# Performance work log

Measured on AMD Instinct MI355X. Metric: run time of the kernel, lower is better.

The kernel has to match this reference:

```python
import math
import jax, jax.numpy as jnp
import numpy as np

D_MODEL = 1024
N_HEAD = 16
HEAD_DIM = D_MODEL // N_HEAD
MAX_LENGTH = 2048


def sinusoid_table():
    # Matches RelativeEmbedding.get_embedding with num_embeddings = max_length + 1
    num_emb = MAX_LENGTH + 1
    half = HEAD_DIM // 2
    freq = jnp.exp(jnp.arange(half, dtype=jnp.float32) * (-math.log(10000.0) / (half - 1)))
    lo = -((num_emb + 1) // 2)  # python floor of -num_emb//2
    hi = num_emb // 2
    pos = jnp.arange(lo, hi, dtype=jnp.float32)  # length num_emb
    ang = pos[:, None] * freq[None, :]
    table = jnp.concatenate([jnp.sin(ang), jnp.cos(ang)], axis=1)  # (num_emb, HEAD_DIM)
    origin_shift = num_emb // 2 + 1
    return table, origin_shift


def _shift(BD):
    # (b, n, L, 2L) -> (b, n, L, L) diagonal-shift trick
    b, n, L, _ = BD.shape
    BD = jnp.concatenate([BD, jnp.zeros((b, n, L, 1), BD.dtype)], axis=-1)
    BD = BD.reshape(b, n, -1, L)[:, :, :-1, :].reshape(b, n, L, -1)
    return BD[:, :, :, :L]


def setup_inputs() -> dict:
    key = jax.random.key(0)
    k1, k2, k3, k4 = jax.random.split(key, 4)
    B, L = 2, 1024
    x = jax.random.normal(k1, (B, L, D_MODEL), dtype=jnp.float32)
    mask = jnp.ones((B, L), dtype=jnp.int32)
    W_qv = jax.random.normal(k2, (2 * D_MODEL, D_MODEL), dtype=jnp.float32) * 0.02
    r_r_bias = jax.random.normal(k3, (N_HEAD, HEAD_DIM), dtype=jnp.float32) * 0.02
    r_w_bias = jax.random.normal(k4, (N_HEAD, HEAD_DIM), dtype=jnp.float32) * 0.02
    return {"x": x, "mask": mask, "W_qv": W_qv, "r_r_bias": r_r_bias, "r_w_bias": r_w_bias}


def reference(x, mask, W_qv, r_r_bias, r_w_bias):
    B, L, d = x.shape
    table, origin_shift = sinusoid_table()
    pos = jnp.arange(-L, L) + origin_shift
    pos_embed = table[pos]  # (2L, head_dim)

    qv = x @ W_qv.T  # (B, L, 2d)
    q, v = jnp.split(qv, 2, axis=-1)
    q = q.reshape(B, L, N_HEAD, HEAD_DIM).transpose(0, 2, 1, 3)  # (B,H,L,dh)
    k = x.reshape(B, L, N_HEAD, HEAD_DIM).transpose(0, 2, 1, 3)
    v = v.reshape(B, L, N_HEAD, HEAD_DIM).transpose(0, 2, 1, 3)

    AC = jnp.einsum('bnqd,bnkd->bnqk', q + r_r_bias[None, :, None, :], k)
    D_ = jnp.einsum('nd,ld->nl', r_w_bias, pos_embed)[None, :, None, :]  # (1,H,1,2L)
    B_ = jnp.einsum('bnqd,ld->bnql', q, pos_embed)  # (B,H,L,2L)
    BD = _shift(B_ + D_)

    attn = AC + BD
    attn = jnp.where(mask[:, None, None, :] == 0, -jnp.inf, attn)
    attn = jax.nn.softmax(attn, axis=-1)
    out = jnp.einsum('bnqk,bnkd->bnqd', attn, v)
    return out.transpose(0, 2, 1, 3).reshape(B, L, d)
```

## Files before the change

### kernel.cpp

```cpp
#include <hip/hip_runtime.h>
#include <hip/hip_bf16.h>
#include <math.h>

#define L_SEQ 1024
#define TWO_L 2048
#define NHEAD 16
#define HD 64
#define DM 1024
#define BATCH 2
#define PE2R 2176
#define GBS 132

typedef _Float16 f16;
typedef _Float16 f16x4 __attribute__((ext_vector_type(4)));
typedef _Float16 f16x8 __attribute__((ext_vector_type(8)));
typedef float f32x4 __attribute__((ext_vector_type(4)));

__device__ __forceinline__ f16x8 ld8(const f16* p) {
  f16x4 lo = *(const f16x4*)p;
  f16x4 hi = *(const f16x4*)(p + 16);
  f16x8 r;
  r[0] = lo[0]; r[1] = lo[1]; r[2] = lo[2]; r[3] = lo[3];
  r[4] = hi[0]; r[5] = hi[1]; r[6] = hi[2]; r[7] = hi[3];
  return r;
}

__device__ __forceinline__ float pe_val(int j, int d) {
  float posval = (float)(j - L_SEQ);
  float freq = expf(-(float)(d & 31) * 0.2971077539347156f);
  float ang = posval * freq;
  return (d < 32) ? sinf(ang) : cosf(ang);
}

__global__ __launch_bounds__(256) void prep1(const float* __restrict__ x,
                                             const float* __restrict__ W,
                                             f16* __restrict__ pe2,
                                             f16* __restrict__ xh,
                                             f16* __restrict__ Wh) {
  int bid = blockIdx.x, tid = threadIdx.x;
  if (bid < 2048) {
    int i = (bid * 256 + tid) * 4;
    float4 v = *(const float4*)(x + i);
    f16x4 o = {(f16)v.x, (f16)v.y, (f16)v.z, (f16)v.w};
    *(f16x4*)(xh + i) = o;
  } else if (bid < 4096) {
    int i = ((bid - 2048) * 256 + tid) * 4;
    float4 v = *(const float4*)(W + i);
    f16x4 o = {(f16)v.x, (f16)v.y, (f16)v.z, (f16)v.w};
    *(f16x4*)(Wh + i) = o;
  } else {
    int idx = (bid - 4096) * 256 + tid;
    int rrow = idx >> 6, d = idx & 63;
    int u = rrow - 1088;
    int j = (u < 0) ? u + 2049 : u;
    float v = (j != 2048) ? pe_val(j, d) : 0.f;
    pe2[idx] = (f16)v;
  }
}

__global__ __launch_bounds__(256) void prep2(const float* __restrict__ rr,
                                             const float* __restrict__ rw,
                                             const f16* __restrict__ pe2,
                                             float* __restrict__ D2x) {
  int idx = blockIdx.x * 256 + threadIdx.x;
  int h = idx / PE2R, r0 = idx - h * PE2R;
  float s = 0.f;
#pragma unroll
  for (int d = 0; d < HD; ++d)
    s = fmaf(rw[h * HD + d] - rr[h * HD + d], (float)pe2[r0 * HD + d], s);
  D2x[idx] = s;
}

#define QV_STEP(T, AS, BS, CA0, CA1, CB0, CB1, NA0, NA1, NB0, NB1)             \
  {                                                                            \
    *(f16x8*)&AS[r * 72 + c] = CA0;                                            \
    *(f16x8*)&AS[r * 72 + c + 8] = CA1;                                        \
    *(f16x8*)&BS[r * 72 + c] = CB0;                                            \
    *(f16x8*)&BS[r * 72 + c + 8] = CB1;                                        \
    __syncthreads();                                                           \
    if ((T) + 1 < 16) {                                                        \
      const f16* na = ga + ((T) + 1) * 64;                                     \
      NA0 = *(const f16x8*)na;                                                 \
      NA1 = *(const f16x8*)(na + 8);                                           \
      const f16* nb = gb + ((T) + 1) * 64;                                     \
      NB0 = *(const f16x8*)nb;                                                 \
      NB1 = *(const f16x8*)(nb + 8);                                           \
    }                                                                          \
    _Pragma("unroll")                                                          \
    for (int kc = 0; kc < 2; ++kc) {                                           \
      f16x8 a = ld8(&AS[(w * 16 + li) * 72 + kc * 32 + g * 4]);                \
      _Pragma("unroll")                                                        \
      for (int nf = 0; nf < 4; ++nf) {                                         \
        f16x8 bfr = ld8(&BS[(nf * 16 + li) * 72 + kc * 32 + g * 4]);           \
        s[nf] = __builtin_amdgcn_mfma_f32_16x16x32_f16(a, bfr, s[nf], 0, 0, 0);\
      }                                                                        \
    }                                                                          \
  }

__global__ __launch_bounds__(256) void qv_mfma(const f16* __restrict__ xh,
                                               const f16* __restrict__ Wh,
                                               f16* __restrict__ qvh,
                                               f16* __restrict__ vT) {
  __shared__ f16 As0[64 * 72], As1[64 * 72];
  __shared__ f16 Bs0[64 * 72], Bs1[64 * 72];
  int tid = threadIdx.x;
  int w = tid >> 6, lane = tid & 63, g = lane >> 4, li = lane & 15;
  int m0 = blockIdx.y * 64, n0 = blockIdx.x * 64;
  int r = tid >> 2, c = (tid & 3) * 16;

  const f16* ga = xh + (size_t)(m0 + r) * 1024 + c;
  const f16* gb = Wh + (size_t)(n0 + r) * 1024 + c;
  f16x8 ca0 = *(const f16x8*)ga, ca1 = *(const f16x8*)(ga + 8);
  f16x8 cb0 = *(const f16x8*)gb, cb1 = *(const f16x8*)(gb + 8);
  f16x8 na0, na1, nb0, nb1;

  f32x4 s[4];
#pragma unroll
  for (int i = 0; i < 4; ++i) s[i] = {0.f, 0.f, 0.f, 0.f};

  for (int t = 0; t < 16; t += 2) {
    QV_STEP(t, As0, Bs0, ca0, ca1, cb0, cb1, na0, na1, nb0, nb1);
    QV_STEP(t + 1, As1, Bs1, na0, na1, nb0, nb1, ca0, ca1, cb0, cb1);
  }

#pragma unroll
  for (int nf = 0; nf < 4; ++nf) {
    int n = n0 + nf * 16 + li;
#pragma unroll
    for (int rr2 = 0; rr2 < 4; ++rr2) {
      int m = m0 + w * 16 + g * 4 + rr2;
      f16 val = (f16)s[nf][rr2];
      if (n < 1024) {
        qvh[(size_t)m * 2048 + n] = val;
      } else {
        int b_ = m >> 10, ls = m & 1023, hd = n - 1024;
        vT[((size_t)(b_ * 16 + (hd >> 6)) * 64 + (hd & 63)) * 1024 + ls] = val;
      }
    }
  }
}

#define BANDFILL(TT, QOFF, PEREG, D2V)                                         \
  {                                                                            \
    _Pragma("unroll")                                                          \
    for (int qf = 0; qf < 4; ++qf) {                                           \
      f32x4 gacc = {0.f, 0.f, 0.f, 0.f};                                       \
      _Pragma("unroll")                                                        \
      for (int kc = 0; kc < 2; ++kc) {                                         \
        f16x8 qo = ld8(&Qs[((QOFF) + qf * 16 + li) * 72 + kc * 32 + g * 4]);   \
        gacc = __builtin_amdgcn_mfma_f32_16x16x32_f16(PEREG[kc], qo, gacc, 0, 0, 0); \
      }                                                                        \
      f16x4 gpk;                                                               \
      gpk[0] = (f16)(gacc[0] + (D2V).x); gpk[1] = (f16)(gacc[1] + (D2V).y);    \
      gpk[2] = (f16)(gacc[2] + (D2V).z); gpk[3] = (f16)(gacc[3] + (D2V).w);    \
      *(f16x4*)&Gb[(qf * 16 + li) * GBS + (TT) + w * 16 + g * 4] = gpk;        \
    }                                                                          \
  }

#define ATTN_STEP(T, CK0, CK1, CV0, CV1, NK0, NK1, NV0, NV1, CPE, NPE)         \
  {                                                                            \
    const int k0 = (T) * 64;                                                   \
    const int tt = (64 * (T)) & 127;                                           \
    const int qoff = (64 * (T) >= q0) ? 1 : 0;                                 \
    *(f16x8*)&Ks[r * 72 + c] = CK0;                                            \
    *(f16x8*)&Ks[r * 72 + c + 8] = CK1;                                        \
    *(f16x8*)&Vs[r * 72 + c] = CV0;                                            \
    *(f16x8*)&Vs[r * 72 + c + 8] = CV1;                                        \
    float4 d2v = *(const float4*)(D2x + hD2 + 1088 + k0 - q0 + w * 16 + g * 4);\
    BANDFILL(tt, qoff, CPE, d2v)                                               \
    __syncthreads();                                                           \
    if ((T) + 1 < 16) {                                                        \
      const f16* nk = gk + (size_t)((T) + 1) * 64 * 1024;                      \
      NK0 = *(const f16x8*)nk;                                                 \
      NK1 = *(const f16x8*)(nk + 8);                                           \
      const f16* nv = gv + ((T) + 1) * 64;                                     \
      NV0 = *(const f16x8*)nv;                                                 \
      NV1 = *(const f16x8*)(nv + 8);                                           \
      const f16* pb = pe2 + (size_t)(1088 + 64 * ((T) + 1) - q0 + w * 16 + li) * 64; \
      NPE[0] = ld8(pb + g * 4);                                                \
      NPE[1] = ld8(pb + 32 + g * 4);                                           \
    }                                                                          \
    float gf[16];                                                              \
    {                                                                          \
      const int cb0 = tt + g * 4 - qi + 128;                                   \
      _Pragma("unroll")                                                        \
      for (int kf = 0; kf < 4; ++kf)                                           \
        _Pragma("unroll")                                                      \
        for (int u2 = 0; u2 < 4; ++u2)                                         \
          gf[kf * 4 + u2] = (float)Gb[qi * GBS + ((cb0 + kf * 16 + u2) & 127)];\
    }                                                                          \
    f32x4 s[4];                                                                \
    _Pragma("unroll")                                                          \
    for (int i = 0; i < 4; ++i) s[i] = {0.f, 0.f, 0.f, 0.f};                   \
    __builtin_amdgcn_s_setprio(1);                                             \
    _Pragma("unroll")                                                          \
    for (int kc = 0; kc < 2; ++kc) {                                           \
      f16x8 qb = ld8(&Qs[(1 + w * 16 + li) * 72 + kc * 32 + g * 4]);           \
      _Pragma("unroll")                                                        \
      for (int kf = 0; kf < 4; ++kf) {                                         \
        f16x8 ka = ld8(&Ks[(kf * 16 + li) * 72 + kc * 32 + g * 4]);            \
        s[kf] = __builtin_amdgcn_mfma_f32_16x16x32_f16(ka, qb, s[kf], 0, 0, 0);\
      }                                                                        \
    }                                                                          \
    __builtin_amdgcn_s_setprio(0);                                             \
    float sv[16];                                                              \
    float tmax = -1e30f;                                                       \
    _Pragma("unroll")                                                          \
    for (int kf = 0; kf < 4; ++kf) {                                           \
      _Pragma("unroll")                                                        \
      for (int rr2 = 0; rr2 < 4; ++rr2) {                                      \
        float v_ = s[kf][rr2] + gf[kf * 4 + rr2] +                             \
                   Ms[k0 + kf * 16 + g * 4 + rr2];                             \
        sv[kf * 4 + rr2] = v_;                                                 \
        tmax = fmaxf(tmax, v_);                                                \
      }                                                                        \
    }                                                                          \
    tmax = fmaxf(tmax, __shfl_xor(tmax, 16));                                  \
    tmax = fmaxf(tmax, __shfl_xor(tmax, 32));                                  \
    if (!__all(tmax <= m_run + 8.f)) {                                         \
      float mnew = fmaxf(m_run, tmax);                                         \
      float scale = __expf(m_run - mnew);                                      \
      m_run = mnew;                                                            \
      l_run *= scale;                                                          \
      _Pragma("unroll")                                                        \
      for (int f = 0; f < 4; ++f) {                                            \
        o[f][0] *= scale; o[f][1] *= scale; o[f][2] *= scale; o[f][3] *= scale;\
      }                                                                        \
    }                                                                          \
    float pf[16];                                                              \
    float lloc = 0.f;                                                          \
    _Pragma("unroll")                                                          \
    for (int i = 0; i < 16; ++i) { pf[i] = __expf(sv[i] - m_run); lloc += pf[i]; } \
    l_run += lloc;                                                             \
    f16x8 pb0, pb1;                                                            \
    _Pragma("unroll")                                                          \
    for (int i = 0; i < 8; ++i) { pb0[i] = (f16)pf[i]; pb1[i] = (f16)pf[8 + i]; } \
    __builtin_amdgcn_s_setprio(1);                                             \
    _Pragma("unroll")                                                          \
    for (int f = 0; f < 4; ++f) {                                              \
      f16x8 va0 = ld8(&Vs[(f * 16 + li) * 72 + g * 4]);                        \
      o[f] = __builtin_amdgcn_mfma_f32_16x16x32_f16(va0, pb0, o[f], 0, 0, 0);  \
      f16x8 va1 = ld8(&Vs[(f * 16 + li) * 72 + 32 + g * 4]);                   \
      o[f] = __builtin_amdgcn_mfma_f32_16x16x32_f16(va1, pb1, o[f], 0, 0, 0);  \
    }                                                                          \
    __builtin_amdgcn_s_setprio(0);                                             \
    __syncthreads();                                                           \
  }

__global__ __launch_bounds__(256) void attn_mfma(const f16* __restrict__ xh,
                                                 const f16* __restrict__ qvh,
                                                 const f16* __restrict__ vT,
                                                 const f16* __restrict__ pe2,
                                                 const float* __restrict__ D2x,
                                                 const int* __restrict__ mask,
                                                 const float* __restrict__ rr,
                                                 float* __restrict__ out) {
  __shared__ f16 Qs[65 * 72];
  __shared__ f16 Ks[64 * 72], Vs[64 * 72];
  __shared__ f16 Gb[64 * GBS];
  __shared__ float Ms[L_SEQ];
  int tid = threadIdx.x;
  int w = tid >> 6, lane = tid & 63, g = lane >> 4, li = lane & 15;
  int bid = blockIdx.x;
  int swz = (bid & 7) * 64 + (bid >> 3);
  int q0 = (swz & 15) * 64;
  int bh = swz >> 4;
  int b = bh >> 4, h = bh & 15;
  int r = tid >> 2, c = (tid & 3) * 16;
  const int qi = w * 16 + li;
  const int hD2 = h * PE2R;

#pragma unroll
  for (int i = 0; i < 4; ++i) {
    int k = tid + i * 256;
    Ms[k] = mask[b * L_SEQ + k] ? 0.f : -1e30f;
  }
  {
    int gq = q0 - 1 + r;
    if (gq < 0) gq = 0;
    const f16* src = qvh + (size_t)(b * L_SEQ + gq) * 2048 + h * HD + c;
#pragma unroll
    for (int u = 0; u < 16; ++u)
      Qs[r * 72 + c + u] = (f16)((float)src[u] + rr[h * HD + c + u]);
    if (tid < 4) {
      int c2 = tid * 16;
      const f16* s2 = qvh + (size_t)(b * L_SEQ + q0 + 63) * 2048 + h * HD + c2;
#pragma unroll
      for (int u = 0; u < 16; ++u)
        Qs[64 * 72 + c2 + u] = (f16)((float)s2[u] + rr[h * HD + c2 + u]);
    }
  }

  const f16* gk = xh + (size_t)(b * L_SEQ + r) * 1024 + h * HD + c;
  const f16* gv = vT + ((size_t)bh * 64 + r) * 1024 + c;
  f16x8 cka = *(const f16x8*)gk, ckb = *(const f16x8*)(gk + 8);
  f16x8 cva = *(const f16x8*)gv, cvb = *(const f16x8*)(gv + 8);
  f16x8 nka, nkb, nva, nvb;
  f16x8 peP[2], peA[2], peB[2];
  {
    const f16* pp = pe2 + (size_t)(1024 - q0 + w * 16 + li) * 64;
    peP[0] = ld8(pp + g * 4);
    peP[1] = ld8(pp + 32 + g * 4);
    const f16* p0 = pe2 + (size_t)(1088 - q0 + w * 16 + li) * 64;
    peA[0] = ld8(p0 + g * 4);
    peA[1] = ld8(p0 + 32 + g * 4);
  }

  __syncthreads();

  {
    float4 d2p = *(const float4*)(D2x + hD2 + 1024 - q0 + w * 16 + g * 4);
    BANDFILL(64, 0, peP, d2p)
  }

  float m_run = -1e30f, l_run = 0.f;
  f32x4 o[4];
#pragma unroll
  for (int i = 0; i < 4; ++i) o[i] = {0.f, 0.f, 0.f, 0.f};

  for (int t = 0; t < 16; t += 2) {
    ATTN_STEP(t, cka, ckb, cva, cvb, nka, nkb, nva, nvb, peA, peB);
    ATTN_STEP(t + 1, nka, nkb, nva, nvb, cka, ckb, cva, cvb, peB, peA);
  }

  float lt = l_run;
  lt += __shfl_xor(lt, 16);
  lt += __shfl_xor(lt, 32);
  float inv = 1.0f / lt;
  int qrow = q0 + qi;
  float* op = out + ((size_t)(b * L_SEQ + qrow)) * DM + h * HD;
#pragma unroll
  for (int f = 0; f < 4; ++f) {
    float4 res = {o[f][0] * inv, o[f][1] * inv, o[f][2] * inv, o[f][3] * inv};
    *(float4*)(op + f * 16 + g * 4) = res;
  }
}

extern "C" void kernel_launch(void* const* d_in, const int* in_sizes, int n_in,
                              void* d_out, int out_size, void* d_ws, size_t ws_size,
                              hipStream_t stream) {
  const float* x = (const float*)d_in[0];
  const int* mask = (const int*)d_in[1];
  const float* W = (const float*)d_in[2];
  const float* rr = (const float*)d_in[3];
  const float* rw = (const float*)d_in[4];
  float* out = (float*)d_out;

  f16* pe2 = (f16*)d_ws;
  float* D2x = (float*)(pe2 + (size_t)PE2R * 64);
  f16* xh = (f16*)(D2x + 16 * PE2R);
  f16* Wh = xh + 2097152;
  f16* qvh = Wh + 2097152;
  f16* vT = qvh + 4194304;

  prep1<<<4096 + (PE2R * 64) / 256, 256, 0, stream>>>(x, W, pe2, xh, Wh);
  prep2<<<(16 * PE2R) / 256, 256, 0, stream>>>(rr, rw, pe2, D2x);
  qv_mfma<<<dim3(32, 32), 256, 0, stream>>>(xh, Wh, qvh, vT);
  attn_mfma<<<512, 256, 0, stream>>>(xh, qvh, vT, pe2, D2x, mask, rr, out);
}
```

Before: 91.87 us.

## Fold prep2 into qv_mfma, hoist Q fragments to registers, skip mask adds

The separate D2x bias kernel is merged into the QV GEMM launch as extra blocks, which removes one kernel launch. In the attention kernel, Q fragments for the QK^T and band-fill MFMAs are loaded once into registers rather than re-read from LDS on every tile. A per-64-key flag built with shared atomics lets fully unmasked tiles skip the mask add. The cost is higher register pressure from the Q fragments and an extra syncthreads plus atomics at kernel start.

```diff
diff --git a/kernel.cpp b/kernel.cpp
--- a/kernel.cpp
+++ b/kernel.cpp
@@ -58,19 +58,6 @@
   }
 }
 
-__global__ __launch_bounds__(256) void prep2(const float* __restrict__ rr,
-                                             const float* __restrict__ rw,
-                                             const f16* __restrict__ pe2,
-                                             float* __restrict__ D2x) {
-  int idx = blockIdx.x * 256 + threadIdx.x;
-  int h = idx / PE2R, r0 = idx - h * PE2R;
-  float s = 0.f;
-#pragma unroll
-  for (int d = 0; d < HD; ++d)
-    s = fmaf(rw[h * HD + d] - rr[h * HD + d], (float)pe2[r0 * HD + d], s);
-  D2x[idx] = s;
-}
-
 #define QV_STEP(T, AS, BS, CA0, CA1, CB0, CB1, NA0, NA1, NB0, NB1)             \
   {                                                                            \
     *(f16x8*)&AS[r * 72 + c] = CA0;                                            \
@@ -100,12 +87,29 @@
 __global__ __launch_bounds__(256) void qv_mfma(const f16* __restrict__ xh,
                                                const f16* __restrict__ Wh,
                                                f16* __restrict__ qvh,
-                                               f16* __restrict__ vT) {
+                                               f16* __restrict__ vT,
+                                               const float* __restrict__ rr,
+                                               const float* __restrict__ rw,
+                                               const f16* __restrict__ pe2,
+                                               float* __restrict__ D2x) {
   __shared__ f16 As0[64 * 72], As1[64 * 72];
   __shared__ f16 Bs0[64 * 72], Bs1[64 * 72];
   int tid = threadIdx.x;
+  int bid = blockIdx.x;
+  if (bid >= 1024) {
+    int idx = (bid - 1024) * 256 + tid;
+    if (idx < 16 * PE2R) {
+      int h = idx / PE2R, r0 = idx - h * PE2R;
+      float s = 0.f;
+#pragma unroll
+      for (int d = 0; d < HD; ++d)
+        s = fmaf(rw[h * HD + d] - rr[h * HD + d], (float)pe2[r0 * HD + d], s);
+      D2x[idx] = s;
+    }
+    return;
+  }
   int w = tid >> 6, lane = tid & 63, g = lane >> 4, li = lane & 15;
-  int m0 = blockIdx.y * 64, n0 = blockIdx.x * 64;
+  int m0 = (bid >> 5) * 64, n0 = (bid & 31) * 64;
   int r = tid >> 2, c = (tid & 3) * 16;
 
   const f16* ga = xh + (size_t)(m0 + r) * 1024 + c;
@@ -145,10 +149,15 @@
     _Pragma("unroll")                                                          \
     for (int qf = 0; qf < 4; ++qf) {                                           \
       f32x4 gacc = {0.f, 0.f, 0.f, 0.f};                                       \
-      _Pragma("unroll")                                                        \
-      for (int kc = 0; kc < 2; ++kc) {                                         \
-        f16x8 qo = ld8(&Qs[((QOFF) + qf * 16 + li) * 72 + kc * 32 + g * 4]);   \
-        gacc = __builtin_amdgcn_mfma_f32_16x16x32_f16(PEREG[kc], qo, gacc, 0, 0, 0); \
+      if (QOFF) {                                                              \
+        gacc = __builtin_amdgcn_mfma_f32_16x16x32_f16(PEREG[0], qB[qf * 2], gacc, 0, 0, 0); \
+        gacc = __builtin_amdgcn_mfma_f32_16x16x32_f16(PEREG[1], qB[qf * 2 + 1], gacc, 0, 0, 0); \
+      } else {                                                                 \
+        _Pragma("unroll")                                                      \
+        for (int kc = 0; kc < 2; ++kc) {                                       \
+          f16x8 qo = ld8(&Qs[(qf * 16 + li) * 72 + kc * 32 + g * 4]);          \
+          gacc = __builtin_amdgcn_mfma_f32_16x16x32_f16(PEREG[kc], qo, gacc, 0, 0, 0); \
+        }                                                                      \
       }                                                                        \
       f16x4 gpk;                                                               \
       gpk[0] = (f16)(gacc[0] + (D2V).x); gpk[1] = (f16)(gacc[1] + (D2V).y);    \
@@ -195,7 +204,7 @@
     __builtin_amdgcn_s_setprio(1);                                             \
     _Pragma("unroll")                                                          \
     for (int kc = 0; kc < 2; ++kc) {                                           \
-      f16x8 qb = ld8(&Qs[(1 + w * 16 + li) * 72 + kc * 32 + g * 4]);           \
+      f16x8 qb = kc ? qk1 : qk0;                                               \
       _Pragma("unroll")                                                        \
       for (int kf = 0; kf < 4; ++kf) {                                         \
         f16x8 ka = ld8(&Ks[(kf * 16 + li) * 72 + kc * 32 + g * 4]);            \
@@ -204,17 +213,22 @@
     }                                                                          \
     __builtin_amdgcn_s_setprio(0);                                             \
     float sv[16];                                                              \
+    _Pragma("unroll")                                                          \
+    for (int kf = 0; kf < 4; ++kf)                                             \
+      _Pragma("unroll")                                                        \
+      for (int rr2 = 0; rr2 < 4; ++rr2)                                        \
+        sv[kf * 4 + rr2] = s[kf][rr2] + gf[kf * 4 + rr2];                      \
+    if (flg[(T)]) {                                                            \
+      _Pragma("unroll")                                                        \
+      for (int kf = 0; kf < 4; ++kf) {                                         \
+        float4 ms4 = *(const float4*)&Ms[k0 + kf * 16 + g * 4];                \
+        sv[kf * 4 + 0] += ms4.x; sv[kf * 4 + 1] += ms4.y;                      \
+        sv[kf * 4 + 2] += ms4.z; sv[kf * 4 + 3] += ms4.w;                      \
+      }                                                                        \
+    }                                                                          \
     float tmax = -1e30f;                                                       \
     _Pragma("unroll")                                                          \
-    for (int kf = 0; kf < 4; ++kf) {                                           \
-      _Pragma("unroll")                                                        \
-      for (int rr2 = 0; rr2 < 4; ++rr2) {                                      \
-        float v_ = s[kf][rr2] + gf[kf * 4 + rr2] +                             \
-                   Ms[k0 + kf * 16 + g * 4 + rr2];                             \
-        sv[kf * 4 + rr2] = v_;                                                 \
-        tmax = fmaxf(tmax, v_);                                                \
-      }                                                                        \
-    }                                                                          \
+    for (int i = 0; i < 16; ++i) tmax = fmaxf(tmax, sv[i]);                    \
     tmax = fmaxf(tmax, __shfl_xor(tmax, 16));                                  \
     tmax = fmaxf(tmax, __shfl_xor(tmax, 32));                                  \
     if (!__all(tmax <= m_run + 8.f)) {                                         \
@@ -259,6 +273,7 @@
   __shared__ f16 Ks[64 * 72], Vs[64 * 72];
   __shared__ f16 Gb[64 * GBS];
   __shared__ float Ms[L_SEQ];
+  __shared__ int flg[16];
   int tid = threadIdx.x;
   int w = tid >> 6, lane = tid & 63, g = lane >> 4, li = lane & 15;
   int bid = blockIdx.x;
@@ -270,10 +285,15 @@
   const int qi = w * 16 + li;
   const int hD2 = h * PE2R;
 
+  if (tid < 16) flg[tid] = 0;
+  __syncthreads();
+
 #pragma unroll
   for (int i = 0; i < 4; ++i) {
     int k = tid + i * 256;
-    Ms[k] = mask[b * L_SEQ + k] ? 0.f : -1e30f;
+    int mv = mask[b * L_SEQ + k];
+    Ms[k] = mv ? 0.f : -1e30f;
+    if (!mv) atomicOr(&flg[k >> 6], 1);
   }
   {
     int gq = q0 - 1 + r;
@@ -308,6 +328,15 @@
 
   __syncthreads();
 
+  f16x8 qk0 = ld8(&Qs[(1 + w * 16 + li) * 72 + g * 4]);
+  f16x8 qk1 = ld8(&Qs[(1 + w * 16 + li) * 72 + 32 + g * 4]);
+  f16x8 qB[8];
+#pragma unroll
+  for (int qf = 0; qf < 4; ++qf) {
+    qB[qf * 2 + 0] = ld8(&Qs[(1 + qf * 16 + li) * 72 + g * 4]);
+    qB[qf * 2 + 1] = ld8(&Qs[(1 + qf * 16 + li) * 72 + 32 + g * 4]);
+  }
+
   {
     float4 d2p = *(const float4*)(D2x + hD2 + 1024 - q0 + w * 16 + g * 4);
     BANDFILL(64, 0, peP, d2p)
@@ -354,7 +383,6 @@
   f16* vT = qvh + 4194304;
 
   prep1<<<4096 + (PE2R * 64) / 256, 256, 0, stream>>>(x, W, pe2, xh, Wh);
-  prep2<<<(16 * PE2R) / 256, 256, 0, stream>>>(rr, rw, pe2, D2x);
-  qv_mfma<<<dim3(32, 32), 256, 0, stream>>>(xh, Wh, qvh, vT);
+  qv_mfma<<<1024 + (16 * PE2R + 255) / 256, 256, 0, stream>>>(xh, Wh, qvh, vT, rr, rw, pe2, D2x);
   attn_mfma<<<512, 256, 0, stream>>>(xh, qvh, vT, pe2, D2x, mask, rr, out);
 }
```

Result: faster. 89.91 us (-2.1%).
